# Kernel tuning notes

Hardware: AMD Instinct MI355X
Metric: run time of the kernel (lower is better)

## Reference

```python
import jax, jax.numpy as jnp
import numpy as np

B, H, S, DK, DV = 2, 16, 2048, 64, 64

def setup_inputs() -> dict:
    key = jax.random.key(0)
    kq, kk, kv, km = jax.random.split(key, 4)
    q = jax.random.normal(kq, (B, H, S, DK), dtype=jnp.float32)
    k = jax.random.normal(kk, (B, H, S, DK), dtype=jnp.float32)
    v = jax.random.normal(kv, (B, H, S, DV), dtype=jnp.float32)
    mask = jax.random.randint(km, (B, H, S, S), 0, 2).astype(jnp.bool_)
    return {"q": q, "k": k, "v": v, "mask": mask}

def reference(q, k, v, mask):
    d_k = q.shape[-1]
    # scores: [B, H, Sq, Sk]
    scores = jnp.einsum('bhqd,bhkd->bhqk', q, k) / np.sqrt(d_k).astype(jnp.float32)
    scores = jnp.where(mask, jnp.float32(-1e9), scores)
    attn = jax.nn.softmax(scores, axis=-1)
    return jnp.einsum('bhqk,bhkd->bhqd', attn, v)
```

## Files before the change

### kernel.cpp

```cpp
#include <hip/hip_runtime.h>


#define LOG2E 1.4426950408889634f
#define QSCALE (0.125f * LOG2E)
#define MASKVAL (-1.0e9f * LOG2E)

typedef __attribute__((ext_vector_type(8))) short short8;
typedef __attribute__((ext_vector_type(4))) float f32x4;

__device__ __forceinline__ short bf16rne(float x) {
  union { float f; unsigned u; } cv; cv.f = x;
  unsigned u = cv.u;
  u += 0x7fffu + ((u >> 16) & 1u);
  return (short)(u >> 16);
}

__global__ void detect_mask_fmt(const unsigned* __restrict__ m, int* __restrict__ flag) {
  unsigned v = m[threadIdx.x];
  unsigned long long isf = __ballot(v == 0x3F800000u);
  unsigned long long big = __ballot(v > 1u);
  if (threadIdx.x == 0) *flag = (isf != 0ull) ? 2 : ((big != 0ull) ? 1 : 0);
}

__launch_bounds__(256)
__global__ void attn_fwd(const float* __restrict__ qp, const float* __restrict__ kp,
                         const float* __restrict__ vp, const void* __restrict__ mp,
                         float* __restrict__ op, const int* __restrict__ fmtp) {
  constexpr int S = 2048, D = 64;
  const int fmt  = *fmtp;
  const int tid  = threadIdx.x;
  const int lane = tid & 63;
  const int w    = tid >> 6;
  const int c    = lane & 15;
  const int quad = lane >> 4;

  const int bh = blockIdx.x >> 5;
  const int q0 = (blockIdx.x & 31) * 64;

  __shared__ short ks[64][72];
  __shared__ short vst[64][72];
  __shared__ short psld[4][16][72];

  const float* qg = qp + ((size_t)(bh * S + q0 + w * 16 + c)) * D;
  short8 qA[2];
#pragma unroll
  for (int kk = 0; kk < 2; ++kk) {
    const float* p = qg + kk * 32 + quad * 8;
    float4 x = *(const float4*)(p);
    float4 y = *(const float4*)(p + 4);
    short8 f;
    f[0] = bf16rne(x.x * QSCALE); f[1] = bf16rne(x.y * QSCALE);
    f[2] = bf16rne(x.z * QSCALE); f[3] = bf16rne(x.w * QSCALE);
    f[4] = bf16rne(y.x * QSCALE); f[5] = bf16rne(y.y * QSCALE);
    f[6] = bf16rne(y.z * QSCALE); f[7] = bf16rne(y.w * QSCALE);
    qA[kk] = f;
  }

  f32x4 O[4];
#pragma unroll
  for (int t = 0; t < 4; ++t) O[t] = (f32x4){0.f, 0.f, 0.f, 0.f};
  float M[4], L[4];
#pragma unroll
  for (int r = 0; r < 4; ++r) { M[r] = -3.0e38f; L[r] = 0.f; }

  const int skey = tid >> 2;
  const int sdb  = (tid & 3) * 16;

  for (int it = 0; it < 32; ++it) {
    const int k0 = it * 64;
    __syncthreads();

    {
      const float* g = kp + ((size_t)(bh * S + k0 + skey)) * D + sdb;
      float4 a = *(const float4*)(g);
      float4 b = *(const float4*)(g + 4);
      float4 e = *(const float4*)(g + 8);
      float4 d = *(const float4*)(g + 12);
      short8 s0, s1;
      s0[0] = bf16rne(a.x); s0[1] = bf16rne(a.y); s0[2] = bf16rne(a.z); s0[3] = bf16rne(a.w);
      s0[4] = bf16rne(b.x); s0[5] = bf16rne(b.y); s0[6] = bf16rne(b.z); s0[7] = bf16rne(b.w);
      s1[0] = bf16rne(e.x); s1[1] = bf16rne(e.y); s1[2] = bf16rne(e.z); s1[3] = bf16rne(e.w);
      s1[4] = bf16rne(d.x); s1[5] = bf16rne(d.y); s1[6] = bf16rne(d.z); s1[7] = bf16rne(d.w);
      *(short8*)&ks[skey][sdb]     = s0;
      *(short8*)&ks[skey][sdb + 8] = s1;
    }
#pragma unroll
    for (int h = 0; h < 2; ++h) {
      int cid = tid + h * 256;
      int dim = cid >> 3;
      int kc  = cid & 7;
      const float* g = vp + ((size_t)(bh * S + k0 + kc * 8)) * D + dim;
      short8 s;
#pragma unroll
      for (int j = 0; j < 8; ++j) s[j] = bf16rne(g[(size_t)j * D]);
      *(short8*)&vst[dim][kc * 8] = s;
    }
    __syncthreads();

    f32x4 Sc[4];
#pragma unroll
    for (int t = 0; t < 4; ++t) {
      short8 b0 = *(const short8*)&ks[t * 16 + c][quad * 8];
      short8 b1 = *(const short8*)&ks[t * 16 + c][32 + quad * 8];
      f32x4 z = (f32x4){0.f, 0.f, 0.f, 0.f};
      z = __builtin_amdgcn_mfma_f32_16x16x32_bf16(qA[0], b0, z, 0, 0, 0);
      z = __builtin_amdgcn_mfma_f32_16x16x32_bf16(qA[1], b1, z, 0, 0, 0);
      Sc[t] = z;
    }

    float tv[4][4];
#pragma unroll
    for (int t = 0; t < 4; ++t)
#pragma unroll
      for (int r = 0; r < 4; ++r) tv[t][r] = Sc[t][r];

    const long long m0 = ((long long)bh * S + (q0 + w * 16 + quad * 4)) * S + k0 + c;
    if (fmt == 1) {
      const unsigned char* mb = (const unsigned char*)mp + m0;
#pragma unroll
      for (int r = 0; r < 4; ++r)
#pragma unroll
        for (int t = 0; t < 4; ++t)
          if (mb[(long long)r * S + t * 16]) tv[t][r] = MASKVAL;
    } else if (fmt == 0) {
      const int* mi = (const int*)mp + m0;
#pragma unroll
      for (int r = 0; r < 4; ++r)
#pragma unroll
        for (int t = 0; t < 4; ++t)
          if (mi[(long long)r * S + t * 16] != 0) tv[t][r] = MASKVAL;
    } else {
      const float* mf = (const float*)mp + m0;
#pragma unroll
      for (int r = 0; r < 4; ++r)
#pragma unroll
        for (int t = 0; t < 4; ++t)
          if (mf[(long long)r * S + t * 16] != 0.f) tv[t][r] = MASKVAL;
    }

    float pm[4];
#pragma unroll
    for (int r = 0; r < 4; ++r)
      pm[r] = fmaxf(fmaxf(tv[0][r], tv[1][r]), fmaxf(tv[2][r], tv[3][r]));
#pragma unroll
    for (int xm = 1; xm < 16; xm <<= 1)
#pragma unroll
      for (int r = 0; r < 4; ++r) pm[r] = fmaxf(pm[r], __shfl_xor(pm[r], xm));

    float al[4];
#pragma unroll
    for (int r = 0; r < 4; ++r) {
      float Mn = fmaxf(M[r], pm[r]);
      al[r] = exp2f(M[r] - Mn);
      M[r] = Mn;
    }
#pragma unroll
    for (int t = 0; t < 4; ++t)
#pragma unroll
      for (int r = 0; r < 4; ++r) tv[t][r] = exp2f(tv[t][r] - M[r]);

    float rs[4];
#pragma unroll
    for (int r = 0; r < 4; ++r)
      rs[r] = (tv[0][r] + tv[1][r]) + (tv[2][r] + tv[3][r]);
#pragma unroll
    for (int xm = 1; xm < 16; xm <<= 1)
#pragma unroll
      for (int r = 0; r < 4; ++r) rs[r] += __shfl_xor(rs[r], xm);

    f32x4 alv = (f32x4){al[0], al[1], al[2], al[3]};
#pragma unroll
    for (int r = 0; r < 4; ++r) L[r] = L[r] * al[r] + rs[r];
#pragma unroll
    for (int t = 0; t < 4; ++t) O[t] *= alv;

#pragma unroll
    for (int r = 0; r < 4; ++r)
#pragma unroll
      for (int t = 0; t < 4; ++t)
        psld[w][quad * 4 + r][t * 16 + c] = bf16rne(tv[t][r]);
    __syncthreads();

    short8 pA0 = *(const short8*)&psld[w][c][quad * 8];
    short8 pA1 = *(const short8*)&psld[w][c][32 + quad * 8];
#pragma unroll
    for (int t = 0; t < 4; ++t) {
      short8 v0 = *(const short8*)&vst[t * 16 + c][quad * 8];
      short8 v1 = *(const short8*)&vst[t * 16 + c][32 + quad * 8];
      O[t] = __builtin_amdgcn_mfma_f32_16x16x32_bf16(pA0, v0, O[t], 0, 0, 0);
      O[t] = __builtin_amdgcn_mfma_f32_16x16x32_bf16(pA1, v1, O[t], 0, 0, 0);
    }
  }

#pragma unroll
  for (int r = 0; r < 4; ++r) {
    float inv = 1.f / L[r];
    const size_t ob = ((size_t)(bh * S + q0 + w * 16 + quad * 4 + r)) * D;
#pragma unroll
    for (int t = 0; t < 4; ++t) op[ob + t * 16 + c] = O[t][r] * inv;
  }
}

extern "C" void kernel_launch(void* const* d_in, const int* in_sizes, int n_in,
                              void* d_out, int out_size, void* d_ws, size_t ws_size,
                              hipStream_t stream) {
  const float* q = (const float*)d_in[0];
  const float* k = (const float*)d_in[1];
  const float* v = (const float*)d_in[2];
  const void*  m = d_in[3];
  int* flag = (int*)d_ws;
  detect_mask_fmt<<<1, 64, 0, stream>>>((const unsigned*)m, flag);
  attn_fwd<<<1024, 256, 0, stream>>>(q, k, v, m, (float*)d_out, flag);
}
```

Before: 821.7 us.

## Pack mask into bitfield and permute key order for contiguous mask reads

Adds a pre-pass kernel that compresses the boolean/int mask into 64-bit ballot words in workspace, so the attention kernel reads one word per row per key tile instead of sixteen scattered byte loads. It also permutes the K/V key order in shared memory so each lane owns four consecutive keys, which lets the fallback path use vector mask loads. A block-wide barrier before the P·V step is dropped, since each wave only reads its own P tile. The cost is an extra full pass over the mask plus a small bit buffer that needs enough workspace; if workspace is too small, the kernel falls back to vectorised direct loads.

```diff
diff --git a/kernel.cpp b/kernel.cpp
--- a/kernel.cpp
+++ b/kernel.cpp
@@ -7,6 +7,11 @@
 
 typedef __attribute__((ext_vector_type(8))) short short8;
 typedef __attribute__((ext_vector_type(4))) float f32x4;
+
+constexpr int S = 2048, D = 64;
+constexpr long long NMASK = 2ll * 16 * 2048 * 2048;
+constexpr long long NWORDS = NMASK / 64;
+constexpr size_t BITS_BYTES = (size_t)NWORDS * 8;
 
 __device__ __forceinline__ short bf16rne(float x) {
   union { float f; unsigned u; } cv; cv.f = x;
@@ -22,12 +27,25 @@
   if (threadIdx.x == 0) *flag = (isf != 0ull) ? 2 : ((big != 0ull) ? 1 : 0);
 }
 
+__global__ void mask_to_bits(const void* __restrict__ mp,
+                             unsigned long long* __restrict__ bits,
+                             const int* __restrict__ fmtp) {
+  const int fmt = *fmtp;
+  const long long gid = (long long)blockIdx.x * 256 + threadIdx.x;
+  unsigned v;
+  if (fmt == 1) v = ((const unsigned char*)mp)[gid];
+  else          v = ((const unsigned*)mp)[gid];
+  unsigned long long b = __ballot(v != 0u);
+  if ((threadIdx.x & 63) == 0) bits[gid >> 6] = b;
+}
+
+template <bool USE_BITS>
 __launch_bounds__(256)
 __global__ void attn_fwd(const float* __restrict__ qp, const float* __restrict__ kp,
                          const float* __restrict__ vp, const void* __restrict__ mp,
+                         const unsigned long long* __restrict__ bitp,
                          float* __restrict__ op, const int* __restrict__ fmtp) {
-  constexpr int S = 2048, D = 64;
-  const int fmt  = *fmtp;
+  const int fmt  = USE_BITS ? 0 : *fmtp;
   const int tid  = threadIdx.x;
   const int lane = tid & 63;
   const int w    = tid >> 6;
@@ -64,7 +82,12 @@
   for (int r = 0; r < 4; ++r) { M[r] = -3.0e38f; L[r] = 0.f; }
 
   const int skey = tid >> 2;
+  const int spos = ((skey & 3) << 4) | (skey >> 2);
   const int sdb  = (tid & 3) * 16;
+
+  const int rq = q0 + w * 16 + quad * 4;
+  const unsigned long long* bmrow =
+      bitp + ((long long)(bh * S + rq)) * (S / 64);
 
   for (int it = 0; it < 32; ++it) {
     const int k0 = it * 64;
@@ -81,19 +104,23 @@
       s0[4] = bf16rne(b.x); s0[5] = bf16rne(b.y); s0[6] = bf16rne(b.z); s0[7] = bf16rne(b.w);
       s1[0] = bf16rne(e.x); s1[1] = bf16rne(e.y); s1[2] = bf16rne(e.z); s1[3] = bf16rne(e.w);
       s1[4] = bf16rne(d.x); s1[5] = bf16rne(d.y); s1[6] = bf16rne(d.z); s1[7] = bf16rne(d.w);
-      *(short8*)&ks[skey][sdb]     = s0;
-      *(short8*)&ks[skey][sdb + 8] = s1;
+      *(short8*)&ks[spos][sdb]     = s0;
+      *(short8*)&ks[spos][sdb + 8] = s1;
     }
 #pragma unroll
     for (int h = 0; h < 2; ++h) {
       int cid = tid + h * 256;
       int dim = cid >> 3;
-      int kc  = cid & 7;
-      const float* g = vp + ((size_t)(bh * S + k0 + kc * 8)) * D + dim;
+      int pb  = (cid & 7) * 8;
+      const float* g = vp + ((size_t)(bh * S + k0)) * D + dim;
       short8 s;
 #pragma unroll
-      for (int j = 0; j < 8; ++j) s[j] = bf16rne(g[(size_t)j * D]);
-      *(short8*)&vst[dim][kc * 8] = s;
+      for (int j = 0; j < 8; ++j) {
+        int pos = pb + j;
+        int key = ((pos & 15) << 2) | (pos >> 4);
+        s[j] = bf16rne(g[(size_t)key * D]);
+      }
+      *(short8*)&vst[dim][pb] = s;
     }
     __syncthreads();
 
@@ -114,28 +141,37 @@
 #pragma unroll
       for (int r = 0; r < 4; ++r) tv[t][r] = Sc[t][r];
 
-    const long long m0 = ((long long)bh * S + (q0 + w * 16 + quad * 4)) * S + k0 + c;
-    if (fmt == 1) {
-      const unsigned char* mb = (const unsigned char*)mp + m0;
-#pragma unroll
-      for (int r = 0; r < 4; ++r)
+    if (USE_BITS) {
+#pragma unroll
+      for (int r = 0; r < 4; ++r) {
+        unsigned long long wv = bmrow[(long long)r * (S / 64) + it];
+        unsigned sh = (unsigned)(wv >> (4 * c));
 #pragma unroll
         for (int t = 0; t < 4; ++t)
-          if (mb[(long long)r * S + t * 16]) tv[t][r] = MASKVAL;
-    } else if (fmt == 0) {
-      const int* mi = (const int*)mp + m0;
-#pragma unroll
-      for (int r = 0; r < 4; ++r)
-#pragma unroll
-        for (int t = 0; t < 4; ++t)
-          if (mi[(long long)r * S + t * 16] != 0) tv[t][r] = MASKVAL;
+          if ((sh >> t) & 1u) tv[t][r] = MASKVAL;
+      }
     } else {
-      const float* mf = (const float*)mp + m0;
-#pragma unroll
-      for (int r = 0; r < 4; ++r)
-#pragma unroll
-        for (int t = 0; t < 4; ++t)
-          if (mf[(long long)r * S + t * 16] != 0.f) tv[t][r] = MASKVAL;
+      const long long m0 = ((long long)(bh * S + rq)) * S + k0 + 4 * c;
+      if (fmt == 1) {
+        const unsigned char* mb = (const unsigned char*)mp + m0;
+#pragma unroll
+        for (int r = 0; r < 4; ++r) {
+          unsigned mv = *(const unsigned*)(mb + (long long)r * S);
+#pragma unroll
+          for (int t = 0; t < 4; ++t)
+            if ((mv >> (8 * t)) & 0xffu) tv[t][r] = MASKVAL;
+        }
+      } else {
+        const unsigned* mi = (const unsigned*)mp + m0;
+#pragma unroll
+        for (int r = 0; r < 4; ++r) {
+          uint4 mv = *(const uint4*)(mi + (long long)r * S);
+          if (mv.x) tv[0][r] = MASKVAL;
+          if (mv.y) tv[1][r] = MASKVAL;
+          if (mv.z) tv[2][r] = MASKVAL;
+          if (mv.w) tv[3][r] = MASKVAL;
+        }
+      }
     }
 
     float pm[4];
@@ -179,7 +215,6 @@
 #pragma unroll
       for (int t = 0; t < 4; ++t)
         psld[w][quad * 4 + r][t * 16 + c] = bf16rne(tv[t][r]);
-    __syncthreads();
 
     short8 pA0 = *(const short8*)&psld[w][c][quad * 8];
     short8 pA1 = *(const short8*)&psld[w][c][32 + quad * 8];
@@ -195,7 +230,7 @@
 #pragma unroll
   for (int r = 0; r < 4; ++r) {
     float inv = 1.f / L[r];
-    const size_t ob = ((size_t)(bh * S + q0 + w * 16 + quad * 4 + r)) * D;
+    const size_t ob = ((size_t)(bh * S + rq + r)) * D;
 #pragma unroll
     for (int t = 0; t < 4; ++t) op[ob + t * 16 + c] = O[t][r] * inv;
   }
@@ -208,7 +243,18 @@
   const float* k = (const float*)d_in[1];
   const float* v = (const float*)d_in[2];
   const void*  m = d_in[3];
-  int* flag = (int*)d_ws;
-  detect_mask_fmt<<<1, 64, 0, stream>>>((const unsigned*)m, flag);
-  attn_fwd<<<1024, 256, 0, stream>>>(q, k, v, m, (float*)d_out, flag);
-}
+
+  unsigned long long* bits = (unsigned long long*)d_ws;
+  int* flag = (int*)((char*)d_ws + BITS_BYTES);
+  const bool use_bits = (ws_size >= BITS_BYTES + 64);
+
+  if (use_bits) {
+    detect_mask_fmt<<<1, 64, 0, stream>>>((const unsigned*)m, flag);
+    mask_to_bits<<<(int)(NMASK / 256), 256, 0, stream>>>(m, bits, flag);
+    attn_fwd<true><<<1024, 256, 0, stream>>>(q, k, v, m, bits, (float*)d_out, flag);
+  } else {
+    int* flag2 = (int*)d_ws;
+    detect_mask_fmt<<<1, 64, 0, stream>>>((const unsigned*)m, flag2);
+    attn_fwd<false><<<1024, 256, 0, stream>>>(q, k, v, m, nullptr, (float*)d_out, flag2);
+  }
+}
```

Measured after the change: 1.025 ms. 1.25x slower.
